# Kernel optimization log

Hardware: AMD Instinct MI355X
Metric: run time of the kernel (lower is better)

## Reference

```python
import jax, jax.numpy as jnp
import numpy as np

TOP_K = 2
N_EXPERTS = 8

def setup_inputs() -> dict:
    key = jax.random.key(0)
    k1, k2, k3, k4 = jax.random.split(key, 4)
    B, C, L, O, E = 8, 4096, 1024, 1024, N_EXPERTS
    scale = 1.0 / np.sqrt(L)
    return {
        "x": jax.random.normal(k1, (B, C, L), dtype=jnp.float32),
        "gate_w": jax.random.normal(k2, (E, L), dtype=jnp.float32) * scale,
        "expert_w": jax.random.normal(k3, (E, O, L), dtype=jnp.float32) * scale,
        "expert_b": jax.random.normal(k4, (E, O), dtype=jnp.float32) * scale,
    }

def reference(x, gate_w, expert_w, expert_b):
    B, C, L = x.shape
    E, O, _ = expert_w.shape
    xt = x.reshape(-1, L)                                  # [T, L], T = B*C
    router_logits = jnp.einsum('tl,el->te', xt, gate_w)    # [T, E]
    probs = jax.nn.softmax(router_logits.astype(jnp.float32), axis=-1)
    routing_weights, selected = jax.lax.top_k(probs, TOP_K)  # [T, K] each
    # combine weight per (token, expert): sum of top-k weights routed to that expert
    comb = jnp.sum(jax.nn.one_hot(selected, E, dtype=routing_weights.dtype)
                   * routing_weights[..., None], axis=1)   # [T, E]
    comb = comb.astype(x.dtype)
    out = jnp.zeros((xt.shape[0], O), dtype=x.dtype)
    for e in range(E):  # small fixed expert loop; masked dense combine
        ye = xt @ expert_w[e].T + expert_b[e]              # [T, O]
        out = out + ye * comb[:, e:e + 1]
    return out.reshape(B, C, O)
```

## Files before the change

### kernel.cpp

```cpp
#include <hip/hip_runtime.h>
#include <cstdint>
#include <cstddef>

#define E_EXP 8
#define LDIM 1024
#define ODIM 1024
#define NPAIR 64

#define BM 256
#define BN 128
#define BK 32
#define NKT (LDIM / BK)
#define MAXRT 160
#define GEMM_GRID (MAXRT * 8)
#define CPX (GEMM_GRID / 8)

typedef __bf16 bf16x8 __attribute__((ext_vector_type(8)));
typedef float f32x4 __attribute__((ext_vector_type(4)));

__device__ __forceinline__ unsigned short f2bf(float f) {
  uint32_t u = __float_as_uint(f);
  u += 0x7FFFu + ((u >> 16) & 1u);
  return (unsigned short)(u >> 16);
}

__device__ __forceinline__ void gload_lds16(const void* g, void* l) {
  __builtin_amdgcn_global_load_lds(
      (const __attribute__((address_space(1))) unsigned int*)g,
      (__attribute__((address_space(3))) unsigned int*)l, 16, 0, 0);
}

__global__ __launch_bounds__(256) void route_kernel(
    const float* __restrict__ x, const float* __restrict__ gate,
    unsigned short* __restrict__ xb, int* __restrict__ sel,
    float2* __restrict__ pw, int T)
{
  const int wid = threadIdx.x >> 6, lane = threadIdx.x & 63;
  const int tok = blockIdx.x * 4 + wid;
  if (tok >= T) return;
  const float* xr = x + (size_t)tok * LDIM;
  unsigned short* xbr = xb + (size_t)tok * LDIM;

  float acc[E_EXP];
#pragma unroll
  for (int e = 0; e < E_EXP; ++e) acc[e] = 0.f;

#pragma unroll
  for (int it = 0; it < 4; ++it) {
    const int c = it * 256 + lane * 4;
    float4 xv = *(const float4*)(xr + c);
    ushort4 bvv;
    bvv.x = f2bf(xv.x); bvv.y = f2bf(xv.y); bvv.z = f2bf(xv.z); bvv.w = f2bf(xv.w);
    *(ushort4*)(xbr + c) = bvv;
#pragma unroll
    for (int e = 0; e < E_EXP; ++e) {
      float4 gv = *(const float4*)(gate + e * LDIM + c);
      acc[e] += xv.x * gv.x + xv.y * gv.y + xv.z * gv.z + xv.w * gv.w;
    }
  }
#pragma unroll
  for (int off = 32; off >= 1; off >>= 1) {
#pragma unroll
    for (int e = 0; e < E_EXP; ++e) acc[e] += __shfl_xor(acc[e], off, 64);
  }
  if (lane == 0) {
    int i1 = 0; float m1 = acc[0];
#pragma unroll
    for (int e = 1; e < E_EXP; ++e) if (acc[e] > m1) { m1 = acc[e]; i1 = e; }
    int i2 = -1; float m2 = -1e30f;
#pragma unroll
    for (int e = 0; e < E_EXP; ++e) if (e != i1 && acc[e] > m2) { m2 = acc[e]; i2 = e; }
    float s = 0.f;
#pragma unroll
    for (int e = 0; e < E_EXP; ++e) s += __expf(acc[e] - m1);
    const float inv = 1.f / s;
    sel[tok] = i1 | (i2 << 4);
    pw[tok] = make_float2(inv, __expf(m2 - m1) * inv);
  }
}

__global__ __launch_bounds__(256) void hist_kernel(
    const int* __restrict__ sel, int* __restrict__ hist2d, int T)
{
  __shared__ int h[NPAIR];
  const int tid = threadIdx.x;
  if (tid < NPAIR) h[tid] = 0;
  __syncthreads();
  const int t0 = blockIdx.x * 2048;
#pragma unroll
  for (int i = 0; i < 8; ++i) {
    const int t = t0 + i * 256 + tid;
    if (t < T) {
      const int s = sel[t];
      const int i1 = s & 15, i2 = (s >> 4) & 15;
      const int lo = i1 < i2 ? i1 : i2, hi = i1 < i2 ? i2 : i1;
      atomicAdd(&h[lo * 8 + hi], 1);
    }
  }
  __syncthreads();
  if (tid < NPAIR) hist2d[blockIdx.x * NPAIR + tid] = h[tid];
}

__global__ void finalize_kernel(
    const int* __restrict__ hist2d, int nb,
    int* __restrict__ blockBase, int4* __restrict__ desc, int* __restrict__ meta)
{
  __shared__ int pcnt[NPAIR], pbase[NPAIR];
  const int p = threadIdx.x;
  if (p < NPAIR) {
    int c = 0;
#pragma unroll 4
    for (int b = 0; b < nb; ++b) c += hist2d[b * NPAIR + p];
    pcnt[p] = c;
  }
  __syncthreads();
  if (p == 0) {
    int s = 0;
    for (int q = 0; q < NPAIR; ++q) { pbase[q] = s; s += pcnt[q]; }
  }
  __syncthreads();
  if (p < NPAIR) {
    int run = pbase[p];
    for (int b = 0; b < nb; ++b) {
      blockBase[b * NPAIR + p] = run;
      run += hist2d[b * NPAIR + p];
    }
  }
  if (p == 0) {
    int rt = 0;
    for (int q = 0; q < NPAIR; ++q) {
      const int lo = q >> 3, hi = q & 7;
      for (int j = 0; j * BM < pcnt[q]; ++j) {
        int rows = pcnt[q] - j * BM; if (rows > BM) rows = BM;
        desc[rt] = make_int4(lo | (hi << 8), pbase[q] + j * BM, rows, 0);
        ++rt;
      }
    }
    meta[0] = rt;
  }
}

__global__ __launch_bounds__(256) void scatter_kernel(
    const int* __restrict__ sel, const float2* __restrict__ pw,
    const int* __restrict__ blockBase, int* __restrict__ tokC,
    float2* __restrict__ wC, int T)
{
  __shared__ int cur[NPAIR];
  const int tid = threadIdx.x;
  if (tid < NPAIR) cur[tid] = blockBase[blockIdx.x * NPAIR + tid];
  __syncthreads();
  const int t0 = blockIdx.x * 2048;
#pragma unroll
  for (int i = 0; i < 8; ++i) {
    const int t = t0 + i * 256 + tid;
    if (t < T) {
      const int s = sel[t];
      const int i1 = s & 15, i2 = (s >> 4) & 15;
      const float2 w = pw[t];
      const int lo = i1 < i2 ? i1 : i2, hi = i1 < i2 ? i2 : i1;
      const float wlo = i1 < i2 ? w.x : w.y;
      const float whi = i1 < i2 ? w.y : w.x;
      const int pos = atomicAdd(&cur[lo * 8 + hi], 1);
      tokC[pos] = t;
      wC[pos] = make_float2(wlo, whi);
    }
  }
}

__global__ __launch_bounds__(256) void convw_kernel(
    const float* __restrict__ w, unsigned short* __restrict__ wb, int n4)
{
  int i = blockIdx.x * 256 + threadIdx.x;
  if (i >= n4) return;
  float4 v = *(const float4*)(w + (size_t)i * 4);
  ushort4 b;
  b.x = f2bf(v.x); b.y = f2bf(v.y); b.z = f2bf(v.z); b.w = f2bf(v.w);
  *(ushort4*)(wb + (size_t)i * 4) = b;
}

__global__ __launch_bounds__(512, 2) void moe_gemm_pair(
    const unsigned short* __restrict__ xb, const unsigned short* __restrict__ wb,
    const float* __restrict__ bias, const int4* __restrict__ desc,
    const int* __restrict__ meta, const int* __restrict__ tokC,
    const float2* __restrict__ wC, float* __restrict__ out)
{
  __shared__ __align__(16) unsigned short ldsA[3][BM * BK];
  __shared__ __align__(16) unsigned short ldsB[3][2 * BN * BK];
  const int tid = threadIdx.x;
  const int lane = tid & 63, w = tid >> 6;
  const int wm = w >> 2, wn = w & 3;

  const int totalRT = meta[0];
  const int swz = ((int)blockIdx.x & 7) * CPX + ((int)blockIdx.x >> 3);
  if (swz >= totalRT * 8) return;
  const int rt = swz >> 3, colTile = swz & 7;
  const int4 d = desc[rt];
  const int lo = d.x & 255, hi = d.x >> 8;
  const int start = d.y, ce = d.z;
  const int* tokL = tokC + start;
  const float2* wgtL = wC + start;

  const int s = lane & 3;
  const int rA0 = w * 32 + (lane >> 2);
  const int rA1 = rA0 + 16;
  const int gA0 = s ^ ((rA0 >> 1) & 3);
  const int gA1 = s ^ ((rA1 >> 1) & 3);
  const int tA0 = tokL[rA0 < ce ? rA0 : ce - 1];
  const int tA1 = tokL[rA1 < ce ? rA1 : ce - 1];
  const char* aSrc0 = (const char*)(xb + (size_t)tA0 * LDIM) + gA0 * 16;
  const char* aSrc1 = (const char*)(xb + (size_t)tA1 * LDIM) + gA1 * 16;
  const int rB = w * 16 + (lane >> 2);
  const int gB = s ^ ((rB >> 1) & 3);
  const int colB = colTile * BN + rB;
  const char* bSrcLo = (const char*)(wb + ((size_t)lo * ODIM + colB) * LDIM) + gB * 16;
  const char* bSrcHi = (const char*)(wb + ((size_t)hi * ODIM + colB) * LDIM) + gB * 16;

  int offA[8], offB[2];
#pragma unroll
  for (int fr = 0; fr < 8; ++fr) {
    const int r = wm * 128 + fr * 16 + (lane & 15);
    offA[fr] = r * BK + (((lane >> 4) ^ ((r >> 1) & 3)) * 8);
  }
#pragma unroll
  for (int fc = 0; fc < 2; ++fc) {
    const int r = wn * 32 + fc * 16 + (lane & 15);
    offB[fc] = r * BK + (((lane >> 4) ^ ((r >> 1) & 3)) * 8);
  }

  auto stage = [&](int b, int kt) {
    const int kb = kt * 64;
    gload_lds16(aSrc0 + kb, &ldsA[b][w * 1024]);
    gload_lds16(aSrc1 + kb, &ldsA[b][w * 1024 + 512]);
    gload_lds16(bSrcLo + kb, &ldsB[b][w * 512]);
    gload_lds16(bSrcHi + kb, &ldsB[b][4096 + w * 512]);
  };

  auto readFrags = [&](int b, bf16x8 (&af)[8], bf16x8 (&bl)[2], bf16x8 (&bh)[2]) {
    const unsigned short* As = &ldsA[b][0];
    const unsigned short* Bs = &ldsB[b][0];
#pragma unroll
    for (int fr = 0; fr < 8; ++fr) af[fr] = *(const bf16x8*)(As + offA[fr]);
#pragma unroll
    for (int fc = 0; fc < 2; ++fc) {
      bl[fc] = *(const bf16x8*)(Bs + offB[fc]);
      bh[fc] = *(const bf16x8*)(Bs + 4096 + offB[fc]);
    }
  };

  f32x4 acc[2][8][2] = {};

  auto mfmaCl = [&](bf16x8 (&af)[8], bf16x8 (&bl)[2], bf16x8 (&bh)[2]) {
#pragma unroll
    for (int fr = 0; fr < 8; ++fr) {
      acc[0][fr][0] = __builtin_amdgcn_mfma_f32_16x16x32_bf16(af[fr], bl[0], acc[0][fr][0], 0, 0, 0);
      acc[0][fr][1] = __builtin_amdgcn_mfma_f32_16x16x32_bf16(af[fr], bl[1], acc[0][fr][1], 0, 0, 0);
      acc[1][fr][0] = __builtin_amdgcn_mfma_f32_16x16x32_bf16(af[fr], bh[0], acc[1][fr][0], 0, 0, 0);
      acc[1][fr][1] = __builtin_amdgcn_mfma_f32_16x16x32_bf16(af[fr], bh[1], acc[1][fr][1], 0, 0, 0);
    }
  };

  bf16x8 afA[8], blA[2], bhA[2], afB[8], blB[2], bhB[2];

  stage(0, 0); stage(1, 1); stage(2, 2);
  asm volatile("s_waitcnt vmcnt(4)" ::: "memory");
  __builtin_amdgcn_s_barrier();
  readFrags(0, afA, blA, bhA);
  asm volatile("s_waitcnt lgkmcnt(0)" ::: "memory");
  __builtin_amdgcn_s_barrier();

#define GEMM_BODY(T_, AFc, BLc, BHc, AFn, BLn, BHn)                          \
  {                                                                          \
    if ((T_) + 3 < NKT) stage((T_) % 3, (T_) + 3);                           \
    if ((T_) + 1 < NKT) readFrags(((T_) + 1) % 3, AFn, BLn, BHn);            \
    mfmaCl(AFc, BLc, BHc);                                                   \
    asm volatile("s_waitcnt lgkmcnt(0)" ::: "memory");                       \
    asm volatile("s_waitcnt vmcnt(4)" ::: "memory");                         \
    __builtin_amdgcn_s_barrier();                                            \
  }

#pragma unroll 1
  for (int t2 = 0; t2 < NKT; t2 += 2) {
    GEMM_BODY(t2,     afA, blA, bhA, afB, blB, bhB);
    GEMM_BODY(t2 + 1, afB, blB, bhB, afA, blA, bhA);
  }
#undef GEMM_BODY

  int cols[2]; float bLo[2], bHi[2];
#pragma unroll
  for (int fc = 0; fc < 2; ++fc) {
    cols[fc] = colTile * BN + wn * 32 + fc * 16 + (lane & 15);
    bLo[fc] = bias[lo * ODIM + cols[fc]];
    bHi[fc] = bias[hi * ODIM + cols[fc]];
  }
#pragma unroll
  for (int fr = 0; fr < 8; ++fr) {
#pragma unroll
    for (int rr = 0; rr < 4; ++rr) {
      const int row = wm * 128 + fr * 16 + (lane >> 4) * 4 + rr;
      if (row < ce) {
        const int tok = tokL[row];
        const float2 ww = wgtL[row];
        float* orow = out + (size_t)tok * ODIM;
#pragma unroll
        for (int fc = 0; fc < 2; ++fc)
          orow[cols[fc]] = ww.x * (acc[0][fr][fc][rr] + bLo[fc]) +
                           ww.y * (acc[1][fr][fc][rr] + bHi[fc]);
      }
    }
  }
}

__global__ __launch_bounds__(256) void naive_moe(
    const float* __restrict__ x, const float* __restrict__ gate,
    const float* __restrict__ ew, const float* __restrict__ eb,
    float* __restrict__ out, int T)
{
  const int tok = blockIdx.x, tid = threadIdx.x;
  __shared__ float xs[LDIM];
  __shared__ float logits[E_EXP];
  __shared__ float sw1, sw2; __shared__ int si1, si2;
  for (int i = tid; i < LDIM; i += 256) xs[i] = x[(size_t)tok * LDIM + i];
  __syncthreads();
  const int wid = tid >> 6, lane = tid & 63;
  for (int e = wid; e < E_EXP; e += 4) {
    float a = 0.f;
    for (int i = lane; i < LDIM; i += 64) a += xs[i] * gate[e * LDIM + i];
    for (int off = 32; off >= 1; off >>= 1) a += __shfl_xor(a, off, 64);
    if (lane == 0) logits[e] = a;
  }
  __syncthreads();
  if (tid == 0) {
    int i1 = 0; float m1 = logits[0];
    for (int e = 1; e < E_EXP; ++e) if (logits[e] > m1) { m1 = logits[e]; i1 = e; }
    int i2 = -1; float m2 = -1e30f;
    for (int e = 0; e < E_EXP; ++e) if (e != i1 && logits[e] > m2) { m2 = logits[e]; i2 = e; }
    float s = 0.f;
    for (int e = 0; e < E_EXP; ++e) s += __expf(logits[e] - m1);
    si1 = i1; si2 = i2; sw1 = 1.f / s; sw2 = __expf(m2 - m1) / s;
  }
  __syncthreads();
  const int i1 = si1, i2 = si2; const float w1 = sw1, w2 = sw2;
  for (int o = tid; o < ODIM; o += 256) {
    float a1 = 0.f, a2 = 0.f;
    const float* p1 = ew + ((size_t)i1 * ODIM + o) * LDIM;
    const float* p2 = ew + ((size_t)i2 * ODIM + o) * LDIM;
    for (int l = 0; l < LDIM; ++l) { a1 += xs[l] * p1[l]; a2 += xs[l] * p2[l]; }
    out[(size_t)tok * ODIM + o] =
        w1 * (a1 + eb[i1 * ODIM + o]) + w2 * (a2 + eb[i2 * ODIM + o]);
  }
}

extern "C" void kernel_launch(void* const* d_in, const int* in_sizes, int n_in,
                              void* d_out, int out_size, void* d_ws, size_t ws_size,
                              hipStream_t stream) {
  const float* x    = (const float*)d_in[0];
  const float* gate = (const float*)d_in[1];
  const float* ew   = (const float*)d_in[2];
  const float* eb   = (const float*)d_in[3];
  float* out = (float*)d_out;
  const int T = in_sizes[0] / LDIM;
  const int NB = (T + 2047) / 2048;

  const size_t offSel   = 0;
  const size_t offPw    = offSel + (size_t)T * 4;
  const size_t offHist  = offPw + (size_t)T * 8;
  const size_t offBBase = offHist + (size_t)NB * NPAIR * 4;
  const size_t offDesc  = offBBase + (size_t)NB * NPAIR * 4;
  const size_t offMeta  = offDesc + (size_t)MAXRT * 16;
  const size_t offTokC  = offMeta + 256;
  const size_t offWC    = offTokC + (size_t)T * 4;
  const size_t offXb    = offWC + (size_t)T * 8;
  const size_t offWb    = offXb + (size_t)T * LDIM * 2;
  const size_t need     = offWb + (size_t)E_EXP * ODIM * LDIM * 2;

  if (ws_size < need) {
    naive_moe<<<T, 256, 0, stream>>>(x, gate, ew, eb, out, T);
    return;
  }

  char* ws = (char*)d_ws;

  route_kernel<<<(T + 3) / 4, 256, 0, stream>>>(
      x, gate, (unsigned short*)(ws + offXb), (int*)(ws + offSel),
      (float2*)(ws + offPw), T);

  const int n4 = E_EXP * ODIM * LDIM / 4;
  convw_kernel<<<(n4 + 255) / 256, 256, 0, stream>>>(ew, (unsigned short*)(ws + offWb), n4);

  hist_kernel<<<NB, 256, 0, stream>>>(
      (const int*)(ws + offSel), (int*)(ws + offHist), T);

  finalize_kernel<<<1, 64, 0, stream>>>(
      (const int*)(ws + offHist), NB, (int*)(ws + offBBase),
      (int4*)(ws + offDesc), (int*)(ws + offMeta));

  scatter_kernel<<<NB, 256, 0, stream>>>(
      (const int*)(ws + offSel), (const float2*)(ws + offPw),
      (const int*)(ws + offBBase), (int*)(ws + offTokC),
      (float2*)(ws + offWC), T);

  moe_gemm_pair<<<GEMM_GRID, 512, 0, stream>>>(
      (const unsigned short*)(ws + offXb), (const unsigned short*)(ws + offWb),
      eb, (const int4*)(ws + offDesc), (const int*)(ws + offMeta),
      (const int*)(ws + offTokC), (const float2*)(ws + offWC), out);
}
```

Measured before the change: 312.6 us.

## Switch GEMM mainloop to double-buffered LDS with in-loop fragment reads and setprio

```diff
diff --git a/kernel.cpp b/kernel.cpp
--- a/kernel.cpp
+++ b/kernel.cpp
@@ -184,8 +184,8 @@
     const int* __restrict__ meta, const int* __restrict__ tokC,
     const float2* __restrict__ wC, float* __restrict__ out)
 {
-  __shared__ __align__(16) unsigned short ldsA[3][BM * BK];
-  __shared__ __align__(16) unsigned short ldsB[3][2 * BN * BK];
+  __shared__ __align__(16) unsigned short ldsA[2][BM * BK];
+  __shared__ __align__(16) unsigned short ldsB[2][2 * BN * BK];
   const int tid = threadIdx.x;
   const int lane = tid & 63, w = tid >> 6;
   const int wm = w >> 2, wn = w & 3;
@@ -235,55 +235,39 @@
     gload_lds16(bSrcHi + kb, &ldsB[b][4096 + w * 512]);
   };
 
-  auto readFrags = [&](int b, bf16x8 (&af)[8], bf16x8 (&bl)[2], bf16x8 (&bh)[2]) {
-    const unsigned short* As = &ldsA[b][0];
-    const unsigned short* Bs = &ldsB[b][0];
-#pragma unroll
-    for (int fr = 0; fr < 8; ++fr) af[fr] = *(const bf16x8*)(As + offA[fr]);
-#pragma unroll
-    for (int fc = 0; fc < 2; ++fc) {
-      bl[fc] = *(const bf16x8*)(Bs + offB[fc]);
-      bh[fc] = *(const bf16x8*)(Bs + 4096 + offB[fc]);
-    }
-  };
-
   f32x4 acc[2][8][2] = {};
 
-  auto mfmaCl = [&](bf16x8 (&af)[8], bf16x8 (&bl)[2], bf16x8 (&bh)[2]) {
-#pragma unroll
-    for (int fr = 0; fr < 8; ++fr) {
-      acc[0][fr][0] = __builtin_amdgcn_mfma_f32_16x16x32_bf16(af[fr], bl[0], acc[0][fr][0], 0, 0, 0);
-      acc[0][fr][1] = __builtin_amdgcn_mfma_f32_16x16x32_bf16(af[fr], bl[1], acc[0][fr][1], 0, 0, 0);
-      acc[1][fr][0] = __builtin_amdgcn_mfma_f32_16x16x32_bf16(af[fr], bh[0], acc[1][fr][0], 0, 0, 0);
-      acc[1][fr][1] = __builtin_amdgcn_mfma_f32_16x16x32_bf16(af[fr], bh[1], acc[1][fr][1], 0, 0, 0);
-    }
-  };
-
-  bf16x8 afA[8], blA[2], bhA[2], afB[8], blB[2], bhB[2];
-
-  stage(0, 0); stage(1, 1); stage(2, 2);
+  stage(0, 0); stage(1, 1);
   asm volatile("s_waitcnt vmcnt(4)" ::: "memory");
   __builtin_amdgcn_s_barrier();
-  readFrags(0, afA, blA, bhA);
-  asm volatile("s_waitcnt lgkmcnt(0)" ::: "memory");
-  __builtin_amdgcn_s_barrier();
-
-#define GEMM_BODY(T_, AFc, BLc, BHc, AFn, BLn, BHn)                          \
-  {                                                                          \
-    if ((T_) + 3 < NKT) stage((T_) % 3, (T_) + 3);                           \
-    if ((T_) + 1 < NKT) readFrags(((T_) + 1) % 3, AFn, BLn, BHn);            \
-    mfmaCl(AFc, BLc, BHc);                                                   \
-    asm volatile("s_waitcnt lgkmcnt(0)" ::: "memory");                       \
-    asm volatile("s_waitcnt vmcnt(4)" ::: "memory");                         \
-    __builtin_amdgcn_s_barrier();                                            \
-  }
 
 #pragma unroll 1
-  for (int t2 = 0; t2 < NKT; t2 += 2) {
-    GEMM_BODY(t2,     afA, blA, bhA, afB, blB, bhB);
-    GEMM_BODY(t2 + 1, afB, blB, bhB, afA, blA, bhA);
-  }
-#undef GEMM_BODY
+  for (int kt = 0; kt < NKT; ++kt) {
+    const int buf = kt & 1;
+    const unsigned short* As = &ldsA[buf][0];
+    const unsigned short* Bs = &ldsB[buf][0];
+    bf16x8 af[8], bl0, bl1, bh0, bh1;
+#pragma unroll
+    for (int fr = 0; fr < 8; ++fr) af[fr] = *(const bf16x8*)(As + offA[fr]);
+    bl0 = *(const bf16x8*)(Bs + offB[0]);
+    bl1 = *(const bf16x8*)(Bs + offB[1]);
+    bh0 = *(const bf16x8*)(Bs + 4096 + offB[0]);
+    bh1 = *(const bf16x8*)(Bs + 4096 + offB[1]);
+    asm volatile("s_waitcnt lgkmcnt(0)" ::: "memory");
+    __builtin_amdgcn_s_barrier();
+    stage(buf, kt + 2 < NKT ? kt + 2 : NKT - 1);
+    __builtin_amdgcn_s_setprio(1);
+#pragma unroll
+    for (int fr = 0; fr < 8; ++fr) {
+      acc[0][fr][0] = __builtin_amdgcn_mfma_f32_16x16x32_bf16(af[fr], bl0, acc[0][fr][0], 0, 0, 0);
+      acc[0][fr][1] = __builtin_amdgcn_mfma_f32_16x16x32_bf16(af[fr], bl1, acc[0][fr][1], 0, 0, 0);
+      acc[1][fr][0] = __builtin_amdgcn_mfma_f32_16x16x32_bf16(af[fr], bh0, acc[1][fr][0], 0, 0, 0);
+      acc[1][fr][1] = __builtin_amdgcn_mfma_f32_16x16x32_bf16(af[fr], bh1, acc[1][fr][1], 0, 0, 0);
+    }
+    __builtin_amdgcn_s_setprio(0);
+    asm volatile("s_waitcnt vmcnt(4)" ::: "memory");
+    __builtin_amdgcn_s_barrier();
+  }
 
   int cols[2]; float bLo[2], bHi[2];
 #pragma unroll
```

New measurement: 287.8 us. 7.9% less time.
